# Performance work log

Measured on AMD Instinct MI355X. Metric: run time of the kernel, lower is better.

## Reference

```python
import jax, jax.numpy as jnp
import numpy as np

IN_DIM = 128
OUT_DIM = 128
GRID_SIZE = 10
SPLINE_ORDER = 3  # k
N_TOKENS = 65536
LN_EPS = 1e-5


def setup_inputs() -> dict:
    key = jax.random.key(0)
    k0, k1, k2 = jax.random.split(key, 3)
    x = jax.random.normal(k0, (N_TOKENS, IN_DIM), dtype=jnp.float32)
    # uniform extended grid on [-1, 1]: [in, grid_size + 2k + 1]
    h = 2.0 / GRID_SIZE
    g1d = jnp.arange(-SPLINE_ORDER, GRID_SIZE + SPLINE_ORDER + 1, dtype=jnp.float32) * h - 1.0
    grid = jnp.tile(g1d[None, :], (IN_DIM, 1))
    base_w = jax.random.normal(k1, (OUT_DIM, IN_DIM), dtype=jnp.float32) / np.float32(np.sqrt(IN_DIM))
    n_coeff = GRID_SIZE + SPLINE_ORDER  # basis functions per input dim
    spline_w = jax.random.normal(k2, (OUT_DIM, IN_DIM * n_coeff), dtype=jnp.float32) * np.float32(0.1 / np.sqrt(IN_DIM))
    gamma = jnp.ones((OUT_DIM,), dtype=jnp.float32)
    beta = jnp.zeros((OUT_DIM,), dtype=jnp.float32)
    return {"x": x, "grid": grid, "base_w": base_w, "spline_w": spline_w, "gamma": gamma, "beta": beta}


def _b_splines(x, grid, k=SPLINE_ORDER):
    # x: [N, in], grid: [in, G+2k+1] -> basis [N, in, G+k] via Cox-de Boor
    xe = x[:, :, None]
    b = ((xe >= grid[:, :-1]) & (xe < grid[:, 1:])).astype(x.dtype)  # order-0
    for p in range(1, k + 1):
        left = (xe - grid[:, : -(p + 1)]) / (grid[:, p:-1] - grid[:, : -(p + 1)]) * b[..., :-1]
        right = (grid[:, p + 1 :] - xe) / (grid[:, p + 1 :] - grid[:, 1:-p]) * b[..., 1:]
        b = left + right
    return b


def reference(x, grid, base_w, spline_w, gamma, beta):
    n = x.shape[0]
    basis = _b_splines(x, grid)  # [N, in, G+k]
    kan = jax.nn.silu(x) @ base_w.T + basis.reshape(n, -1) @ spline_w.T  # [N, out]
    # LayerNorm over last dim
    mu = jnp.mean(kan, axis=-1, keepdims=True)
    var = jnp.mean(jnp.square(kan - mu), axis=-1, keepdims=True)
    out = (kan - mu) * jax.lax.rsqrt(var + LN_EPS) * gamma + beta
    # dropout is identity in eval mode; skip = Identity since in_dim == out_dim
    return out + x
```

## Files before the change

### kernel.cpp

```cpp
#include <hip/hip_runtime.h>


#define DIM 128
#define NCOEFF 13
#define SLOT 16
#define KTOT (DIM * SLOT)
#define DPC 8
#define KC (DPC * SLOT)
#define NCHUNK (DIM / DPC)
#define MTILE 64
#define ABUF (MTILE * DPC * SLOT)
#define WB_BYTES (DIM * KTOT * 2)

typedef __attribute__((ext_vector_type(8))) short short8;
typedef __attribute__((ext_vector_type(8))) __bf16 bf16x8;
typedef __attribute__((ext_vector_type(4))) float f32x4;
typedef __attribute__((ext_vector_type(2))) unsigned long long u64x2;

__device__ __forceinline__ unsigned short f2bf(float f) {
  unsigned int u = __builtin_bit_cast(unsigned int, f);
  u += 0x7fffu + ((u >> 16) & 1u);
  return (unsigned short)(u >> 16);
}

__global__ void kan_prep_wfrag(const float* __restrict__ base_w,
                               const float* __restrict__ spline_w,
                               unsigned short* __restrict__ Wf) {
  int u = blockIdx.x * 256 + threadIdx.x;
  int lane = u & 63;
  int blk = u >> 6;
  int ntile = blk & 7;
  int khi = blk >> 3;
  int q = lane >> 4, ln = lane & 15;
  int n = ntile * 16 + ln;
  int k0 = khi * 32 + q * 8;
  unsigned short v[8];
#pragma unroll
  for (int j = 0; j < 8; ++j) {
    int k = k0 + j;
    int i = k >> 4, s = k & 15;
    float f = (s == 0) ? base_w[n * DIM + i]
            : (s <= 13 ? spline_w[n * (DIM * NCOEFF) + i * NCOEFF + (s - 1)] : 0.f);
    v[j] = f2bf(f);
  }
  short8 pack;
#pragma unroll
  for (int j = 0; j < 8; ++j) pack[j] = (short)v[j];
  ((short8*)Wf)[u] = pack;
}

__device__ __forceinline__ void build_slots(float xv, unsigned long long r[4]) {
  float sil = xv * __builtin_amdgcn_rcpf(1.0f + __expf(-xv));
  float tp = (xv + 1.6f) * 5.0f;
  int m = (int)floorf(tp);
  bool valid = (xv >= -1.6f) && (xv < 1.6f);
  m = m < 0 ? 0 : (m > 15 ? 15 : m);
  float u = tp - (float)m;
  float omu = 1.0f - u;
  float w0 = 0.166666667f * omu * omu * omu;
  float w3 = 0.166666667f * u * u * u;
  float w1 = (0.5f * u - 1.0f) * u * u + 0.666666667f;
  float w2 = (0.5f * omu - 1.0f) * omu * omu + 0.666666667f;
  unsigned long long W =
      (unsigned long long)f2bf(w0) |
      ((unsigned long long)f2bf(w1) << 16) |
      ((unsigned long long)f2bf(w2) << 32) |
      ((unsigned long long)f2bf(w3) << 48);
  if (!valid) W = 0;
  int p = m - 2;
#pragma unroll
  for (int j = 0; j < 4; ++j) {
    int d = 64 * j - 16 * p;
    unsigned long long rj;
    if (d >= 64 || d <= -64) rj = 0;
    else if (d >= 0) rj = W >> d;
    else rj = W << (-d);
    r[j] = rj;
  }
  r[0] = (r[0] & ~0xFFFFULL) | (unsigned long long)f2bf(sil);
  r[3] &= 0xFFFFFFFFULL;
}

__device__ __forceinline__ int a_off(int t, int i, int h) {
  return (((i >> 1) * 4 + (t >> 4)) << 9) + ((((i & 1) * 2 + h) << 4) + (t & 15)) * 8;
}

__device__ __forceinline__ void stage_elem(unsigned short* Ab, int t, int i, float xv) {
  unsigned long long r[4];
  build_slots(xv, r);
  *(short8*)(Ab + a_off(t, i, 0)) = __builtin_bit_cast(short8, (u64x2){r[0], r[1]});
  *(short8*)(Ab + a_off(t, i, 1)) = __builtin_bit_cast(short8, (u64x2){r[2], r[3]});
}

template <bool BF16W>
__global__ __launch_bounds__(256, 4)
void kan_fused(const float* __restrict__ x,
               const unsigned short* __restrict__ Wf,
               const float* __restrict__ base_w,
               const float* __restrict__ spline_w,
               const float* __restrict__ gamma,
               const float* __restrict__ beta,
               float* __restrict__ out) {
  __shared__ __align__(16) unsigned short A_lds[2][ABUF];
  __shared__ float S1p[4][MTILE];
  __shared__ float S2p[4][MTILE];

  const int tid = threadIdx.x;
  const int lane = tid & 63, wave = tid >> 6;
  const int q = lane >> 4, ln = lane & 15;
  const long tokBase = (long)blockIdx.x * MTILE;

  f32x4 acc[4][2];
#pragma unroll
  for (int a = 0; a < 4; ++a)
#pragma unroll
    for (int b = 0; b < 2; ++b) acc[a][b] = (f32x4){0.f, 0.f, 0.f, 0.f};

  const int il = tid & 7;
  const int tr0 = tid >> 3;

  {
    float xv0 = x[(tokBase + tr0) * DIM + il];
    float xv1 = x[(tokBase + tr0 + 32) * DIM + il];
    stage_elem(A_lds[0], tr0, il, xv0);
    stage_elem(A_lds[0], tr0 + 32, il, xv1);
  }
  short8 bfr[4][2];
#pragma unroll
  for (int ks = 0; ks < 4; ++ks)
#pragma unroll
    for (int nt = 0; nt < 2; ++nt) {
      if (BF16W) {
        bfr[ks][nt] = *(const short8*)(Wf + ((ks * 8) + wave * 2 + nt) * 512 + lane * 8);
      } else {
        const int n = wave * 32 + nt * 16 + ln;
        const int kg = ks * 32 + q * 8;
        float f[8];
        int i = kg >> 4, s0 = kg & 15;
        if (s0 == 0) {
          f[0] = base_w[n * DIM + i];
#pragma unroll
          for (int j = 0; j < 7; ++j) f[1 + j] = spline_w[n * (DIM * NCOEFF) + i * NCOEFF + j];
        } else {
#pragma unroll
          for (int j = 0; j < 6; ++j) f[j] = spline_w[n * (DIM * NCOEFF) + i * NCOEFF + 7 + j];
          f[6] = 0.f; f[7] = 0.f;
        }
        short8 tmp;
#pragma unroll
        for (int j = 0; j < 8; ++j) tmp[j] = (short)f2bf(f[j]);
        bfr[ks][nt] = tmp;
      }
    }

  for (int c = 0; c < NCHUNK; ++c) {
    __syncthreads();
    float xv0 = 0.f, xv1 = 0.f;
    if (c + 1 < NCHUNK) {
      const float* xc = x + (c + 1) * DPC + il;
      xv0 = xc[(tokBase + tr0) * DIM];
      xv1 = xc[(tokBase + tr0 + 32) * DIM];
    }
    const unsigned short* Ab = A_lds[c & 1];
#pragma unroll
    for (int ks = 0; ks < 4; ++ks) {
      short8 af[4];
#pragma unroll
      for (int mt = 0; mt < 4; ++mt)
        af[mt] = *(const short8*)&Ab[((ks * 4 + mt) << 9) + lane * 8];
#pragma unroll
      for (int mt = 0; mt < 4; ++mt)
#pragma unroll
        for (int nt = 0; nt < 2; ++nt)
          acc[mt][nt] = __builtin_amdgcn_mfma_f32_16x16x32_bf16(
              __builtin_bit_cast(bf16x8, af[mt]), __builtin_bit_cast(bf16x8, bfr[ks][nt]),
              acc[mt][nt], 0, 0, 0);
    }
    if (c + 1 < NCHUNK) {
#pragma unroll
      for (int ks = 0; ks < 4; ++ks)
#pragma unroll
        for (int nt = 0; nt < 2; ++nt) {
          if (BF16W) {
            bfr[ks][nt] = *(const short8*)(Wf + (((c + 1) * 4 + ks) * 8 + wave * 2 + nt) * 512 + lane * 8);
          } else {
            const int n = wave * 32 + nt * 16 + ln;
            const int kg = (c + 1) * KC + ks * 32 + q * 8;
            float f[8];
            int i = kg >> 4, s0 = kg & 15;
            if (s0 == 0) {
              f[0] = base_w[n * DIM + i];
#pragma unroll
              for (int j = 0; j < 7; ++j) f[1 + j] = spline_w[n * (DIM * NCOEFF) + i * NCOEFF + j];
            } else {
#pragma unroll
              for (int j = 0; j < 6; ++j) f[j] = spline_w[n * (DIM * NCOEFF) + i * NCOEFF + 7 + j];
              f[6] = 0.f; f[7] = 0.f;
            }
            short8 tmp;
#pragma unroll
            for (int j = 0; j < 8; ++j) tmp[j] = (short)f2bf(f[j]);
            bfr[ks][nt] = tmp;
          }
        }
      unsigned short* Bb = A_lds[(c + 1) & 1];
      stage_elem(Bb, tr0, il, xv0);
      stage_elem(Bb, tr0 + 32, il, xv1);
    }
  }

#pragma unroll
  for (int mt = 0; mt < 4; ++mt) {
#pragma unroll
    for (int r = 0; r < 4; ++r) {
      float s1 = 0.f, s2 = 0.f;
#pragma unroll
      for (int nt = 0; nt < 2; ++nt) { float v = acc[mt][nt][r]; s1 += v; s2 += v * v; }
#pragma unroll
      for (int off = 1; off < 16; off <<= 1) {
        s1 += __shfl_xor(s1, off);
        s2 += __shfl_xor(s2, off);
      }
      if (ln == 0) {
        int t = mt * 16 + q * 4 + r;
        S1p[wave][t] = s1;
        S2p[wave][t] = s2;
      }
    }
  }
  __syncthreads();
  float gv[2], bv[2];
#pragma unroll
  for (int nt = 0; nt < 2; ++nt) {
    int n = wave * 32 + nt * 16 + ln;
    gv[nt] = gamma[n];
    bv[nt] = beta[n];
  }
#pragma unroll
  for (int mt = 0; mt < 4; ++mt) {
#pragma unroll
    for (int r = 0; r < 4; ++r) {
      int t = mt * 16 + q * 4 + r;
      float s1 = S1p[0][t] + S1p[1][t] + S1p[2][t] + S1p[3][t];
      float s2 = S2p[0][t] + S2p[1][t] + S2p[2][t] + S2p[3][t];
      float mean = s1 * (1.0f / 128.0f);
      float var = s2 * (1.0f / 128.0f) - mean * mean;
      float inv = __builtin_amdgcn_rsqf(var + 1e-5f);
      long rowo = (tokBase + t) * DIM;
#pragma unroll
      for (int nt = 0; nt < 2; ++nt) {
        int n = wave * 32 + nt * 16 + ln;
        float o = (acc[mt][nt][r] - mean) * inv * gv[nt] + bv[nt] + x[rowo + n];
        out[rowo + n] = o;
      }
    }
  }
}

extern "C" void kernel_launch(void* const* d_in, const int* in_sizes, int n_in,
                              void* d_out, int out_size, void* d_ws, size_t ws_size,
                              hipStream_t stream) {
  const float* x        = (const float*)d_in[0];
  const float* base_w   = (const float*)d_in[2];
  const float* spline_w = (const float*)d_in[3];
  const float* gamma    = (const float*)d_in[4];
  const float* beta     = (const float*)d_in[5];
  float* out = (float*)d_out;

  const int n_tokens = in_sizes[0] / DIM;
  const int nblocks = n_tokens / MTILE;

  if (ws_size >= (size_t)WB_BYTES) {
    unsigned short* Wf = (unsigned short*)d_ws;
    kan_prep_wfrag<<<(DIM * KTOT / 8) / 256, 256, 0, stream>>>(base_w, spline_w, Wf);
    kan_fused<true><<<nblocks, 256, 0, stream>>>(x, Wf, base_w, spline_w, gamma, beta, out);
  } else {
    kan_fused<false><<<nblocks, 256, 0, stream>>>(x, nullptr, base_w, spline_w, gamma, beta, out);
  }
}
```

Before: 139.5 us.

## Prefetch x two chunks ahead through LDS and pair-vectorize spline basis build

Global x loads become coalesced float2 reads issued two chunks ahead and parked in a padded LDS transpose buffer. Each thread then builds basis slots for two input dims at once using packed float2 math. The main loop is unrolled by two so the buffers are addressed statically. The bf16 packing now truncates instead of rounding to nearest even, using perm, which cuts ALU work but slightly changes numerics. The intent is to hide global load latency and lower VALU cost in the staging phase, at the price of extra LDS and more complex indexing.

```diff
diff --git a/kernel.cpp b/kernel.cpp
--- a/kernel.cpp
+++ b/kernel.cpp
@@ -10,11 +10,13 @@
 #define NCHUNK (DIM / DPC)
 #define MTILE 64
 #define ABUF (MTILE * DPC * SLOT)
+#define XSTR 68
 #define WB_BYTES (DIM * KTOT * 2)
 
 typedef __attribute__((ext_vector_type(8))) short short8;
 typedef __attribute__((ext_vector_type(8))) __bf16 bf16x8;
 typedef __attribute__((ext_vector_type(4))) float f32x4;
+typedef __attribute__((ext_vector_type(2))) float f32x2;
 typedef __attribute__((ext_vector_type(2))) unsigned long long u64x2;
 
 __device__ __forceinline__ unsigned short f2bf(float f) {
@@ -49,23 +51,14 @@
   ((short8*)Wf)[u] = pack;
 }
 
-__device__ __forceinline__ void build_slots(float xv, unsigned long long r[4]) {
-  float sil = xv * __builtin_amdgcn_rcpf(1.0f + __expf(-xv));
-  float tp = (xv + 1.6f) * 5.0f;
-  int m = (int)floorf(tp);
-  bool valid = (xv >= -1.6f) && (xv < 1.6f);
-  m = m < 0 ? 0 : (m > 15 ? 15 : m);
-  float u = tp - (float)m;
-  float omu = 1.0f - u;
-  float w0 = 0.166666667f * omu * omu * omu;
-  float w3 = 0.166666667f * u * u * u;
-  float w1 = (0.5f * u - 1.0f) * u * u + 0.666666667f;
-  float w2 = (0.5f * omu - 1.0f) * omu * omu + 0.666666667f;
-  unsigned long long W =
-      (unsigned long long)f2bf(w0) |
-      ((unsigned long long)f2bf(w1) << 16) |
-      ((unsigned long long)f2bf(w2) << 32) |
-      ((unsigned long long)f2bf(w3) << 48);
+__device__ __forceinline__ void finish_elem(float w0, float w1, float w2, float w3,
+                                            float sil, int m, bool valid,
+                                            unsigned long long r[4]) {
+  unsigned int lo = __builtin_amdgcn_perm(__builtin_bit_cast(unsigned int, w1),
+                                          __builtin_bit_cast(unsigned int, w0), 0x07060302u);
+  unsigned int hi = __builtin_amdgcn_perm(__builtin_bit_cast(unsigned int, w3),
+                                          __builtin_bit_cast(unsigned int, w2), 0x07060302u);
+  unsigned long long W = ((unsigned long long)hi << 32) | lo;
   if (!valid) W = 0;
   int p = m - 2;
 #pragma unroll
@@ -77,19 +70,128 @@
     else rj = W << (-d);
     r[j] = rj;
   }
-  r[0] = (r[0] & ~0xFFFFULL) | (unsigned long long)f2bf(sil);
+  unsigned int sb = __builtin_bit_cast(unsigned int, sil) >> 16;
+  r[0] = (r[0] & ~0xFFFFULL) | (unsigned long long)sb;
   r[3] &= 0xFFFFFFFFULL;
+}
+
+__device__ __forceinline__ void build_slots_pair(f32x2 xv,
+                                                 unsigned long long ra[4],
+                                                 unsigned long long rb[4]) {
+  f32x2 sig;
+  sig.x = __builtin_amdgcn_rcpf(1.0f + __expf(-xv.x));
+  sig.y = __builtin_amdgcn_rcpf(1.0f + __expf(-xv.y));
+  f32x2 sil = xv * sig;
+  f32x2 tp = (xv + 1.6f) * 5.0f;
+  float mf0 = floorf(tp.x), mf1 = floorf(tp.y);
+  int m0 = (int)mf0, m1 = (int)mf1;
+  bool v0 = (xv.x >= -1.6f) && (xv.x < 1.6f);
+  bool v1 = (xv.y >= -1.6f) && (xv.y < 1.6f);
+  m0 = m0 < 0 ? 0 : (m0 > 15 ? 15 : m0);
+  m1 = m1 < 0 ? 0 : (m1 > 15 ? 15 : m1);
+  f32x2 mc = {(float)m0, (float)m1};
+  f32x2 u = tp - mc;
+  f32x2 omu = 1.0f - u;
+  f32x2 u2 = u * u, o2 = omu * omu;
+  f32x2 w0 = (0.166666667f * o2) * omu;
+  f32x2 w3 = (0.166666667f * u2) * u;
+  f32x2 w1 = (0.5f * u - 1.0f) * u2 + 0.666666667f;
+  f32x2 w2 = (0.5f * omu - 1.0f) * o2 + 0.666666667f;
+  finish_elem(w0.x, w1.x, w2.x, w3.x, sil.x, m0, v0, ra);
+  finish_elem(w0.y, w1.y, w2.y, w3.y, sil.y, m1, v1, rb);
 }
 
 __device__ __forceinline__ int a_off(int t, int i, int h) {
   return (((i >> 1) * 4 + (t >> 4)) << 9) + ((((i & 1) * 2 + h) << 4) + (t & 15)) * 8;
 }
 
-__device__ __forceinline__ void stage_elem(unsigned short* Ab, int t, int i, float xv) {
-  unsigned long long r[4];
-  build_slots(xv, r);
-  *(short8*)(Ab + a_off(t, i, 0)) = __builtin_bit_cast(short8, (u64x2){r[0], r[1]});
-  *(short8*)(Ab + a_off(t, i, 1)) = __builtin_bit_cast(short8, (u64x2){r[2], r[3]});
+__device__ __forceinline__ void stage_pair(unsigned short* Ab, int ts, int i2, f32x2 xs) {
+  unsigned long long ra[4], rb[4];
+  build_slots_pair(xs, ra, rb);
+  *(short8*)(Ab + a_off(ts, i2, 0)) = __builtin_bit_cast(short8, (u64x2){ra[0], ra[1]});
+  *(short8*)(Ab + a_off(ts, i2, 1)) = __builtin_bit_cast(short8, (u64x2){ra[2], ra[3]});
+  *(short8*)(Ab + a_off(ts, i2 + 4, 0)) = __builtin_bit_cast(short8, (u64x2){rb[0], rb[1]});
+  *(short8*)(Ab + a_off(ts, i2 + 4, 1)) = __builtin_bit_cast(short8, (u64x2){rb[2], rb[3]});
+}
+
+template <bool BF16W>
+__device__ __forceinline__ void load_bfr(const unsigned short* __restrict__ Wf,
+                                         const float* __restrict__ base_w,
+                                         const float* __restrict__ spline_w,
+                                         int c, int wave, int lane, int q, int ln,
+                                         short8 (&bfr)[4][2]) {
+#pragma unroll
+  for (int ks = 0; ks < 4; ++ks)
+#pragma unroll
+    for (int nt = 0; nt < 2; ++nt) {
+      if (BF16W) {
+        bfr[ks][nt] = *(const short8*)(Wf + ((c * 4 + ks) * 8 + wave * 2 + nt) * 512 + lane * 8);
+      } else {
+        const int n = wave * 32 + nt * 16 + ln;
+        const int kg = c * KC + ks * 32 + q * 8;
+        float f[8];
+        int i = kg >> 4, s0 = kg & 15;
+        if (s0 == 0) {
+          f[0] = base_w[n * DIM + i];
+#pragma unroll
+          for (int j = 0; j < 7; ++j) f[1 + j] = spline_w[n * (DIM * NCOEFF) + i * NCOEFF + j];
+        } else {
+#pragma unroll
+          for (int j = 0; j < 6; ++j) f[j] = spline_w[n * (DIM * NCOEFF) + i * NCOEFF + 7 + j];
+          f[6] = 0.f; f[7] = 0.f;
+        }
+        short8 tmp;
+#pragma unroll
+        for (int j = 0; j < 8; ++j) tmp[j] = (short)f2bf(f[j]);
+        bfr[ks][nt] = tmp;
+      }
+    }
+}
+
+template <bool BF16W>
+__device__ __forceinline__ void chunk_body(int c,
+    const float* __restrict__ x, const unsigned short* __restrict__ Wf,
+    const float* __restrict__ base_w, const float* __restrict__ spline_w,
+    unsigned short* curA, unsigned short* nxtA,
+    const float* xsrc, float* xdst,
+    short8 (&bfr)[4][2], f32x4 (&acc)[4][2],
+    long tokBase, int tid) {
+  const int lane = tid & 63, wave = tid >> 6;
+  const int q = lane >> 4, ln = lane & 15;
+  const int iw2 = (tid & 3) * 2;
+  const int t2 = tid >> 2;
+  const int ts = tid & 63;
+  const int i2 = tid >> 6;
+
+  __syncthreads();
+  f32x2 xg = {0.f, 0.f};
+  if (c + 2 < NCHUNK)
+    xg = *(const f32x2*)&x[(tokBase + t2) * DIM + (c + 2) * DPC + iw2];
+#pragma unroll
+  for (int ks = 0; ks < 4; ++ks) {
+    short8 af[4];
+#pragma unroll
+    for (int mt = 0; mt < 4; ++mt)
+      af[mt] = *(const short8*)&curA[((ks * 4 + mt) << 9) + lane * 8];
+#pragma unroll
+    for (int mt = 0; mt < 4; ++mt)
+#pragma unroll
+      for (int nt = 0; nt < 2; ++nt)
+        acc[mt][nt] = __builtin_amdgcn_mfma_f32_16x16x32_bf16(
+            __builtin_bit_cast(bf16x8, af[mt]), __builtin_bit_cast(bf16x8, bfr[ks][nt]),
+            acc[mt][nt], 0, 0, 0);
+  }
+  if (c + 1 < NCHUNK) {
+    load_bfr<BF16W>(Wf, base_w, spline_w, c + 1, wave, lane, q, ln, bfr);
+    f32x2 xs;
+    xs.x = xsrc[i2 * XSTR + ts];
+    xs.y = xsrc[(i2 + 4) * XSTR + ts];
+    stage_pair(nxtA, ts, i2, xs);
+  }
+  if (c + 2 < NCHUNK) {
+    xdst[iw2 * XSTR + t2] = xg.x;
+    xdst[(iw2 + 1) * XSTR + t2] = xg.y;
+  }
 }
 
 template <bool BF16W>
@@ -102,12 +204,17 @@
                const float* __restrict__ beta,
                float* __restrict__ out) {
   __shared__ __align__(16) unsigned short A_lds[2][ABUF];
+  __shared__ float x_lds[2][DPC * XSTR];
   __shared__ float S1p[4][MTILE];
   __shared__ float S2p[4][MTILE];
 
   const int tid = threadIdx.x;
   const int lane = tid & 63, wave = tid >> 6;
   const int q = lane >> 4, ln = lane & 15;
+  const int iw2 = (tid & 3) * 2;
+  const int t2 = tid >> 2;
+  const int ts = tid & 63;
+  const int i2 = tid >> 6;
   const long tokBase = (long)blockIdx.x * MTILE;
 
   f32x4 acc[4][2];
@@ -116,97 +223,23 @@
 #pragma unroll
     for (int b = 0; b < 2; ++b) acc[a][b] = (f32x4){0.f, 0.f, 0.f, 0.f};
 
-  const int il = tid & 7;
-  const int tr0 = tid >> 3;
-
   {
-    float xv0 = x[(tokBase + tr0) * DIM + il];
-    float xv1 = x[(tokBase + tr0 + 32) * DIM + il];
-    stage_elem(A_lds[0], tr0, il, xv0);
-    stage_elem(A_lds[0], tr0 + 32, il, xv1);
+    f32x2 x0;
+    x0.x = x[(tokBase + ts) * DIM + i2];
+    x0.y = x[(tokBase + ts) * DIM + i2 + 4];
+    stage_pair(A_lds[0], ts, i2, x0);
+    f32x2 f0 = *(const f32x2*)&x[(tokBase + t2) * DIM + DPC + iw2];
+    x_lds[1][iw2 * XSTR + t2] = f0.x;
+    x_lds[1][(iw2 + 1) * XSTR + t2] = f0.y;
   }
   short8 bfr[4][2];
-#pragma unroll
-  for (int ks = 0; ks < 4; ++ks)
-#pragma unroll
-    for (int nt = 0; nt < 2; ++nt) {
-      if (BF16W) {
-        bfr[ks][nt] = *(const short8*)(Wf + ((ks * 8) + wave * 2 + nt) * 512 + lane * 8);
-      } else {
-        const int n = wave * 32 + nt * 16 + ln;
-        const int kg = ks * 32 + q * 8;
-        float f[8];
-        int i = kg >> 4, s0 = kg & 15;
-        if (s0 == 0) {
-          f[0] = base_w[n * DIM + i];
-#pragma unroll
-          for (int j = 0; j < 7; ++j) f[1 + j] = spline_w[n * (DIM * NCOEFF) + i * NCOEFF + j];
-        } else {
-#pragma unroll
-          for (int j = 0; j < 6; ++j) f[j] = spline_w[n * (DIM * NCOEFF) + i * NCOEFF + 7 + j];
-          f[6] = 0.f; f[7] = 0.f;
-        }
-        short8 tmp;
-#pragma unroll
-        for (int j = 0; j < 8; ++j) tmp[j] = (short)f2bf(f[j]);
-        bfr[ks][nt] = tmp;
-      }
-    }
-
-  for (int c = 0; c < NCHUNK; ++c) {
-    __syncthreads();
-    float xv0 = 0.f, xv1 = 0.f;
-    if (c + 1 < NCHUNK) {
-      const float* xc = x + (c + 1) * DPC + il;
-      xv0 = xc[(tokBase + tr0) * DIM];
-      xv1 = xc[(tokBase + tr0 + 32) * DIM];
-    }
-    const unsigned short* Ab = A_lds[c & 1];
-#pragma unroll
-    for (int ks = 0; ks < 4; ++ks) {
-      short8 af[4];
-#pragma unroll
-      for (int mt = 0; mt < 4; ++mt)
-        af[mt] = *(const short8*)&Ab[((ks * 4 + mt) << 9) + lane * 8];
-#pragma unroll
-      for (int mt = 0; mt < 4; ++mt)
-#pragma unroll
-        for (int nt = 0; nt < 2; ++nt)
-          acc[mt][nt] = __builtin_amdgcn_mfma_f32_16x16x32_bf16(
-              __builtin_bit_cast(bf16x8, af[mt]), __builtin_bit_cast(bf16x8, bfr[ks][nt]),
-              acc[mt][nt], 0, 0, 0);
-    }
-    if (c + 1 < NCHUNK) {
-#pragma unroll
-      for (int ks = 0; ks < 4; ++ks)
-#pragma unroll
-        for (int nt = 0; nt < 2; ++nt) {
-          if (BF16W) {
-            bfr[ks][nt] = *(const short8*)(Wf + (((c + 1) * 4 + ks) * 8 + wave * 2 + nt) * 512 + lane * 8);
-          } else {
-            const int n = wave * 32 + nt * 16 + ln;
-            const int kg = (c + 1) * KC + ks * 32 + q * 8;
-            float f[8];
-            int i = kg >> 4, s0 = kg & 15;
-            if (s0 == 0) {
-              f[0] = base_w[n * DIM + i];
-#pragma unroll
-              for (int j = 0; j < 7; ++j) f[1 + j] = spline_w[n * (DIM * NCOEFF) + i * NCOEFF + j];
-            } else {
-#pragma unroll
-              for (int j = 0; j < 6; ++j) f[j] = spline_w[n * (DIM * NCOEFF) + i * NCOEFF + 7 + j];
-              f[6] = 0.f; f[7] = 0.f;
-            }
-            short8 tmp;
-#pragma unroll
-            for (int j = 0; j < 8; ++j) tmp[j] = (short)f2bf(f[j]);
-            bfr[ks][nt] = tmp;
-          }
-        }
-      unsigned short* Bb = A_lds[(c + 1) & 1];
-      stage_elem(Bb, tr0, il, xv0);
-      stage_elem(Bb, tr0 + 32, il, xv1);
-    }
+  load_bfr<BF16W>(Wf, base_w, spline_w, 0, wave, lane, q, ln, bfr);
+
+  for (int cc = 0; cc < NCHUNK; cc += 2) {
+    chunk_body<BF16W>(cc,     x, Wf, base_w, spline_w, A_lds[0], A_lds[1],
+                      x_lds[1], x_lds[0], bfr, acc, tokBase, tid);
+    chunk_body<BF16W>(cc + 1, x, Wf, base_w, spline_w, A_lds[1], A_lds[0],
+                      x_lds[0], x_lds[1], bfr, acc, tokBase, tid);
   }
 
 #pragma unroll
```

Result: faster. 126.6 us (-9.3%).
